# Kernel optimization log

Measured on AMD Instinct MI355X. Metric: run time of the kernel, lower is better.

The kernel has to match this reference:

```python
import jax, jax.numpy as jnp
import numpy as np

HEADS = 4
DIM_HEAD = 128

def setup_inputs() -> dict:
    key = jax.random.key(0)
    k1, k2, k3, k4 = jax.random.split(key, 4)
    scale = DIM_HEAD ** -0.5
    return {
        "fmap": jax.random.normal(k1, (16, 512, 32, 32), dtype=jnp.float32),
        "w_qkv": jax.random.normal(k2, (1536, 512), dtype=jnp.float32) * 0.02,
        "height": jax.random.normal(k3, (32, DIM_HEAD), dtype=jnp.float32) * scale,
        "width": jax.random.normal(k4, (32, DIM_HEAD), dtype=jnp.float32) * scale,
    }

def reference(fmap, w_qkv, height, width):
    b, c, h, w = fmap.shape
    scale = DIM_HEAD ** -0.5
    # 1x1 conv == channel GEMM: (b, 3*heads*dim_head, h, w)
    qkv = jnp.einsum('bchw,oc->bohw', fmap, w_qkv)
    # split into q,k,v and reshape to (b, heads, seq, dim_head)
    qkv = qkv.reshape(b, 3, HEADS, DIM_HEAD, h * w)
    q, k, v = (jnp.transpose(qkv[:, i], (0, 1, 3, 2)) for i in range(3))
    # content logits
    sim = jnp.einsum('bhid,bhjd->bhij', q, k) * scale
    # absolute positional bias: emb[(x,y)] = height[x] + width[y]
    emb = (height[:, None, :] + width[None, :, :]).reshape(h * w, DIM_HEAD)
    sim = sim + jnp.einsum('bhid,jd->bhij', q, emb) * scale
    attn = jax.nn.softmax(sim, axis=-1)
    out = jnp.einsum('bhij,bhjd->bhid', attn, v)  # (b, heads, seq, d)
    out = jnp.transpose(out, (0, 1, 3, 2)).reshape(b, HEADS * DIM_HEAD, h, w)
    return out
```

## Files before the change

kernel.cpp:

```cpp
#include <hip/hip_runtime.h>
#include <math.h>

#define HEADS 4
#define DIMH  128
#define NB    16
#define CIN   512
#define SEQ   1024
#define OTOT  1536

typedef __attribute__((ext_vector_type(8)))  short bf16x8;
typedef __attribute__((ext_vector_type(4)))  short bf16x4;
typedef __attribute__((ext_vector_type(4)))  float f32x4;
typedef __attribute__((ext_vector_type(16))) float f32x16;

#define MFMA16(a,b,c) __builtin_amdgcn_mfma_f32_16x16x32_bf16(a,b,c,0,0,0)
#define MFMA32(a,b,c) __builtin_amdgcn_mfma_f32_32x32x16_bf16(a,b,c,0,0,0)

#define GLOAD16(g, s) __builtin_amdgcn_global_load_lds( \
    (const __attribute__((address_space(1))) unsigned int*)(g), \
    (__attribute__((address_space(3))) unsigned int*)(s), 16, 0, 0)

__device__ __forceinline__ short f2bf(float f) {
    unsigned u = __builtin_bit_cast(unsigned, f);
    u = (u + 0x7FFFu + ((u >> 16) & 1u)) >> 16;
    return (short)u;
}

__global__ __launch_bounds__(256) void convert_fmap(const float* __restrict__ F,
                                                    short* __restrict__ FT) {
    __shared__ float tile[32][33];
    const int b = blockIdx.z, c0 = blockIdx.y * 32, s0 = blockIdx.x * 32;
    const int t = threadIdx.x;
    #pragma unroll
    for (int p = 0; p < 4; ++p) {
        int c = (t >> 5) + p * 8, s = t & 31;
        tile[c][s] = F[((size_t)b * CIN + c0 + c) * SEQ + s0 + s];
    }
    __syncthreads();
    #pragma unroll
    for (int p = 0; p < 2; ++p) {
        int s = (t >> 4) + p * 16, c2 = (t & 15) * 2;
        unsigned lo = (unsigned short)f2bf(tile[c2][s]);
        unsigned hi = (unsigned short)f2bf(tile[c2 + 1][s]);
        *(unsigned*)&FT[((size_t)b * SEQ + s0 + s) * CIN + c0 + c2] = lo | (hi << 16);
    }
}

__global__ __launch_bounds__(256) void convert_w(const float* __restrict__ W,
                                                 short* __restrict__ Wb) {
    int i = (blockIdx.x * 256 + threadIdx.x) * 4;
    float4 v = *(const float4*)&W[i];
    bf16x4 pk = { f2bf(v.x), f2bf(v.y), f2bf(v.z), f2bf(v.w) };
    *(bf16x4*)&Wb[i] = pk;
}

__global__ __launch_bounds__(256) void qkv_gemm(
    const short* __restrict__ Wb, const short* __restrict__ FT,
    const float* __restrict__ height, const float* __restrict__ width,
    short* __restrict__ Qo, short* __restrict__ Ko, short* __restrict__ Vo)
{
    __shared__ short As[128 * 32];
    __shared__ short Bs[128 * 32];
    const int b = blockIdx.z, o0 = blockIdx.y * 128, s0 = blockIdx.x * 128;
    const int t = threadIdx.x, l = t & 63, w = t >> 6;
    const int quad = l >> 4, ln = l & 15;
    const int wrow = (w >> 1) * 64, wcol = (w & 1) * 64;

    const short* Ablk = Wb + (size_t)o0 * CIN;
    const short* Bblk = FT + ((size_t)b * SEQ + s0) * CIN;

    f32x4 acc[4][4] = {};

    const int lrow = l >> 2, lcol = (l & 3) * 8;

    for (int k0 = 0; k0 < CIN; k0 += 32) {
        __syncthreads();
        {
            const short* gA = Ablk + (size_t)(w * 32 + lrow) * CIN + k0 + lcol;
            GLOAD16(gA,            As + (w * 32) * 32);
            GLOAD16(gA + 16 * CIN, As + (w * 32 + 16) * 32);
            const short* gB = Bblk + (size_t)(w * 32 + lrow) * CIN + k0 + lcol;
            GLOAD16(gB,            Bs + (w * 32) * 32);
            GLOAD16(gB + 16 * CIN, Bs + (w * 32 + 16) * 32);
        }
        __syncthreads();
        bf16x8 af[4], bfr[4];
        #pragma unroll
        for (int i = 0; i < 4; ++i)
            af[i] = *(const bf16x8*)&As[(wrow + i * 16 + ln) * 32 + quad * 8];
        #pragma unroll
        for (int j = 0; j < 4; ++j)
            bfr[j] = *(const bf16x8*)&Bs[(wcol + j * 16 + ln) * 32 + quad * 8];
        #pragma unroll
        for (int i = 0; i < 4; ++i)
            #pragma unroll
            for (int j = 0; j < 4; ++j)
                acc[i][j] = MFMA16(af[i], bfr[j], acc[i][j]);
    }

    const int sec = o0 >> 9;
    const int h   = (o0 >> 7) & 3;
    const size_t bh = (size_t)b * HEADS + h;

    if (sec == 0) {
        const float qs = 0.08838834764831845f * 1.4426950408889634f;
        #pragma unroll
        for (int ti = 0; ti < 4; ++ti) {
            int d = wrow + ti * 16 + quad * 4;
            #pragma unroll
            for (int tj = 0; tj < 4; ++tj) {
                int s = s0 + wcol + tj * 16 + ln;
                f32x4 a = acc[ti][tj];
                bf16x4 pk = { f2bf(a[0] * qs), f2bf(a[1] * qs), f2bf(a[2] * qs), f2bf(a[3] * qs) };
                *(bf16x4*)&Qo[(bh * SEQ + s) * DIMH + d] = pk;
            }
        }
    } else if (sec == 1) {
        #pragma unroll
        for (int ti = 0; ti < 4; ++ti) {
            int d = wrow + ti * 16 + quad * 4;
            #pragma unroll
            for (int tj = 0; tj < 4; ++tj) {
                int s = s0 + wcol + tj * 16 + ln;
                float4 hv = *(const float4*)&height[(size_t)(s >> 5) * DIMH + d];
                float4 wv = *(const float4*)&width[(size_t)(s & 31) * DIMH + d];
                f32x4 a = acc[ti][tj];
                bf16x4 pk = { f2bf(a[0] + hv.x + wv.x), f2bf(a[1] + hv.y + wv.y),
                              f2bf(a[2] + hv.z + wv.z), f2bf(a[3] + hv.w + wv.w) };
                *(bf16x4*)&Ko[(bh * SEQ + s) * DIMH + d] = pk;
            }
        }
    } else {
        #pragma unroll
        for (int ti = 0; ti < 4; ++ti) {
            int d = wrow + ti * 16 + quad * 4;
            #pragma unroll
            for (int tj = 0; tj < 4; ++tj) {
                int s = s0 + wcol + tj * 16 + ln;
                f32x4 a = acc[ti][tj];
                #pragma unroll
                for (int r = 0; r < 4; ++r)
                    Vo[(bh * DIMH + d + r) * SEQ + s] = f2bf(a[r]);
            }
        }
    }
}

#define BQ 128
#define BJ 64
#define KSTR 136
#define VSTR 72
#define PSTR 72

__global__ __launch_bounds__(256, 2) void attn(
    const short* __restrict__ Q, const short* __restrict__ K,
    const short* __restrict__ V, float* __restrict__ out)
{
    __shared__ short Ks[BJ * KSTR];
    __shared__ short Vs[DIMH * VSTR];
    __shared__ short Ps[BQ * PSTR];
    __shared__ float ls[BQ];

    const int t = threadIdx.x, l = t & 63, w = t >> 6;
    const int h = l >> 5, c31 = l & 31;

    const int L = blockIdx.x;
    const int x = L & 7, inner = L >> 3;
    const int bh = x * 8 + (inner >> 3);
    const int q0 = (inner & 7) * BQ;
    const size_t base = (size_t)bh * DIMH * SEQ;

    bf16x8 qf[8];
    {
        const short* Qp = Q + base + (size_t)(q0 + w * 32 + c31) * DIMH + h * 8;
        #pragma unroll
        for (int kc = 0; kc < 8; ++kc)
            qf[kc] = *(const bf16x8*)(Qp + kc * 16);
    }

    f32x16 O[4] = {};
    f32x16 psum = {};

    for (int j0 = 0; j0 < SEQ; j0 += BJ) {
        __syncthreads();
        #pragma unroll
        for (int p = 0; p < 4; ++p) {
            int j = (w * 4 + p) * 4 + (l >> 4);
            int c8 = (l & 15) * 8;
            int4 v = *(const int4*)(K + base + (size_t)(j0 + j) * DIMH + c8);
            *(int4*)&Ks[j * KSTR + c8] = v;
        }
        #pragma unroll
        for (int p = 0; p < 4; ++p) {
            int d = (w * 4 + p) * 8 + (l >> 3);
            int j8 = (l & 7) * 8;
            int4 v = *(const int4*)(V + base + (size_t)d * SEQ + j0 + j8);
            *(int4*)&Vs[d * VSTR + j8] = v;
        }
        __syncthreads();

        f32x16 S0 = {}, S1 = {};
        #pragma unroll
        for (int kc = 0; kc < 8; ++kc) {
            bf16x8 k0 = *(const bf16x8*)&Ks[c31 * KSTR + kc * 16 + h * 8];
            bf16x8 k1 = *(const bf16x8*)&Ks[(32 + c31) * KSTR + kc * 16 + h * 8];
            S0 = MFMA32(qf[kc], k0, S0);
            S1 = MFMA32(qf[kc], k1, S1);
        }

        #pragma unroll
        for (int r = 0; r < 16; ++r) {
            float p0 = __builtin_amdgcn_exp2f(S0[r]);
            float p1 = __builtin_amdgcn_exp2f(S1[r]);
            psum[r] += p0 + p1;
            int i = w * 32 + (r & 3) + 8 * (r >> 2) + 4 * h;
            Ps[i * PSTR + c31]      = f2bf(p0);
            Ps[i * PSTR + 32 + c31] = f2bf(p1);
        }

        #pragma unroll
        for (int jc = 0; jc < 4; ++jc) {
            bf16x8 pf = *(const bf16x8*)&Ps[(w * 32 + c31) * PSTR + jc * 16 + h * 8];
            #pragma unroll
            for (int dc = 0; dc < 4; ++dc) {
                bf16x8 vf = *(const bf16x8*)&Vs[(dc * 32 + c31) * VSTR + jc * 16 + h * 8];
                O[dc] = MFMA32(vf, pf, O[dc]);
            }
        }
    }

    #pragma unroll
    for (int r = 0; r < 16; ++r) {
        float s = psum[r];
        #pragma unroll
        for (int m = 1; m < 32; m <<= 1) s += __shfl_xor(s, m);
        psum[r] = s;
    }
    if (c31 == 0) {
        #pragma unroll
        for (int r = 0; r < 16; ++r)
            ls[w * 32 + (r & 3) + 8 * (r >> 2) + 4 * h] = psum[r];
    }
    float linv = 1.0f / ls[w * 32 + c31];

    #pragma unroll
    for (int dc = 0; dc < 4; ++dc)
        #pragma unroll
        for (int r = 0; r < 16; ++r) {
            int d = dc * 32 + (r & 3) + 8 * (r >> 2) + 4 * h;
            out[base + (size_t)d * SEQ + q0 + w * 32 + c31] = O[dc][r] * linv;
        }
}

extern "C" void kernel_launch(void* const* d_in, const int* in_sizes, int n_in,
                              void* d_out, int out_size, void* d_ws, size_t ws_size,
                              hipStream_t stream) {
    const float* fmap   = (const float*)d_in[0];
    const float* w_qkv  = (const float*)d_in[1];
    const float* height = (const float*)d_in[2];
    const float* width  = (const float*)d_in[3];
    float* outp = (float*)d_out;

    const size_t n_ft  = (size_t)NB * SEQ * CIN;
    const size_t n_w   = (size_t)OTOT * CIN;
    const size_t n_qkv = (size_t)NB * HEADS * SEQ * DIMH;

    short* FT = (short*)d_ws;
    short* Wb = FT + n_ft;
    short* Qb = Wb + n_w;
    short* Kb = Qb + n_qkv;
    short* Vb = Kb + n_qkv;

    convert_fmap<<<dim3(SEQ / 32, CIN / 32, NB), 256, 0, stream>>>(fmap, FT);
    convert_w<<<dim3(n_w / 1024), 256, 0, stream>>>(w_qkv, Wb);
    qkv_gemm<<<dim3(SEQ / 128, OTOT / 128, NB), 256, 0, stream>>>(
        Wb, FT, height, width, Qb, Kb, Vb);
    attn<<<dim3(NB * HEADS * (SEQ / BQ)), 256, 0, stream>>>(Qb, Kb, Vb, outp);
}
```

Baseline: 183.7 us.

## Pre-pack GEMM operands in k-octet layout and load MFMA fragments directly from global

The fmap and weight conversion kernels now write bf16 data in a [k/8][row][8] interleaved layout, so each lane's MFMA fragment is one contiguous 16-byte global load. The QKV GEMM drops its LDS staging and barriers and reads fragments straight from global memory, with a launch-bounds occupancy hint and a partially unrolled k loop. This removes LDS traffic and the two syncs per k-step. The cost is no data reuse through shared memory, so every wave fetches its own A/B fragments from L2 or HBM. Latency hiding now depends on occupancy and the unrolling alone.

Result: faster. 177.9 us (-3.2%).

```diff
diff --git a/kernel.cpp b/kernel.cpp
--- a/kernel.cpp
+++ b/kernel.cpp
@@ -7,6 +7,7 @@
 #define CIN   512
 #define SEQ   1024
 #define OTOT  1536
+#define KQ    (CIN / 8)
 
 typedef __attribute__((ext_vector_type(8)))  short bf16x8;
 typedef __attribute__((ext_vector_type(4)))  short bf16x4;
@@ -16,81 +17,60 @@
 #define MFMA16(a,b,c) __builtin_amdgcn_mfma_f32_16x16x32_bf16(a,b,c,0,0,0)
 #define MFMA32(a,b,c) __builtin_amdgcn_mfma_f32_32x32x16_bf16(a,b,c,0,0,0)
 
-#define GLOAD16(g, s) __builtin_amdgcn_global_load_lds( \
-    (const __attribute__((address_space(1))) unsigned int*)(g), \
-    (__attribute__((address_space(3))) unsigned int*)(s), 16, 0, 0)
-
 __device__ __forceinline__ short f2bf(float f) {
     unsigned u = __builtin_bit_cast(unsigned, f);
     u = (u + 0x7FFFu + ((u >> 16) & 1u)) >> 16;
     return (short)u;
 }
 
+__global__ __launch_bounds__(256) void convert_w(const float* __restrict__ W,
+                                                 short* __restrict__ Wb2) {
+    const int o  = blockIdx.x * 256 + threadIdx.x;
+    const int kq = blockIdx.y;
+    float4 v0 = *(const float4*)&W[(size_t)o * CIN + kq * 8];
+    float4 v1 = *(const float4*)&W[(size_t)o * CIN + kq * 8 + 4];
+    bf16x8 pk = { f2bf(v0.x), f2bf(v0.y), f2bf(v0.z), f2bf(v0.w),
+                  f2bf(v1.x), f2bf(v1.y), f2bf(v1.z), f2bf(v1.w) };
+    *(bf16x8*)&Wb2[((size_t)kq * OTOT + o) * 8] = pk;
+}
+
 __global__ __launch_bounds__(256) void convert_fmap(const float* __restrict__ F,
-                                                    short* __restrict__ FT) {
-    __shared__ float tile[32][33];
-    const int b = blockIdx.z, c0 = blockIdx.y * 32, s0 = blockIdx.x * 32;
-    const int t = threadIdx.x;
+                                                    short* __restrict__ FT2) {
+    const int s  = blockIdx.x * 256 + threadIdx.x;
+    const int kq = blockIdx.y, b = blockIdx.z;
+    const float* src = F + ((size_t)b * CIN + kq * 8) * SEQ + s;
+    float v[8];
     #pragma unroll
-    for (int p = 0; p < 4; ++p) {
-        int c = (t >> 5) + p * 8, s = t & 31;
-        tile[c][s] = F[((size_t)b * CIN + c0 + c) * SEQ + s0 + s];
-    }
-    __syncthreads();
-    #pragma unroll
-    for (int p = 0; p < 2; ++p) {
-        int s = (t >> 4) + p * 16, c2 = (t & 15) * 2;
-        unsigned lo = (unsigned short)f2bf(tile[c2][s]);
-        unsigned hi = (unsigned short)f2bf(tile[c2 + 1][s]);
-        *(unsigned*)&FT[((size_t)b * SEQ + s0 + s) * CIN + c0 + c2] = lo | (hi << 16);
-    }
-}
-
-__global__ __launch_bounds__(256) void convert_w(const float* __restrict__ W,
-                                                 short* __restrict__ Wb) {
-    int i = (blockIdx.x * 256 + threadIdx.x) * 4;
-    float4 v = *(const float4*)&W[i];
-    bf16x4 pk = { f2bf(v.x), f2bf(v.y), f2bf(v.z), f2bf(v.w) };
-    *(bf16x4*)&Wb[i] = pk;
-}
-
-__global__ __launch_bounds__(256) void qkv_gemm(
-    const short* __restrict__ Wb, const short* __restrict__ FT,
+    for (int i = 0; i < 8; ++i) v[i] = src[(size_t)i * SEQ];
+    bf16x8 pk = { f2bf(v[0]), f2bf(v[1]), f2bf(v[2]), f2bf(v[3]),
+                  f2bf(v[4]), f2bf(v[5]), f2bf(v[6]), f2bf(v[7]) };
+    *(bf16x8*)&FT2[(((size_t)b * KQ + kq) * SEQ + s) * 8] = pk;
+}
+
+__global__ __launch_bounds__(256, 3) void qkv_gemm(
+    const short* __restrict__ Wb2, const short* __restrict__ FT2,
     const float* __restrict__ height, const float* __restrict__ width,
     short* __restrict__ Qo, short* __restrict__ Ko, short* __restrict__ Vo)
 {
-    __shared__ short As[128 * 32];
-    __shared__ short Bs[128 * 32];
     const int b = blockIdx.z, o0 = blockIdx.y * 128, s0 = blockIdx.x * 128;
     const int t = threadIdx.x, l = t & 63, w = t >> 6;
     const int quad = l >> 4, ln = l & 15;
     const int wrow = (w >> 1) * 64, wcol = (w & 1) * 64;
 
-    const short* Ablk = Wb + (size_t)o0 * CIN;
-    const short* Bblk = FT + ((size_t)b * SEQ + s0) * CIN;
+    const short* Ap = Wb2 + (((size_t)quad * OTOT) + (o0 + wrow + ln)) * 8;
+    const short* Bp = FT2 + ((((size_t)b * KQ + quad) * SEQ) + (s0 + wcol + ln)) * 8;
 
     f32x4 acc[4][4] = {};
 
-    const int lrow = l >> 2, lcol = (l & 3) * 8;
-
-    for (int k0 = 0; k0 < CIN; k0 += 32) {
-        __syncthreads();
-        {
-            const short* gA = Ablk + (size_t)(w * 32 + lrow) * CIN + k0 + lcol;
-            GLOAD16(gA,            As + (w * 32) * 32);
-            GLOAD16(gA + 16 * CIN, As + (w * 32 + 16) * 32);
-            const short* gB = Bblk + (size_t)(w * 32 + lrow) * CIN + k0 + lcol;
-            GLOAD16(gB,            Bs + (w * 32) * 32);
-            GLOAD16(gB + 16 * CIN, Bs + (w * 32 + 16) * 32);
-        }
-        __syncthreads();
+    #pragma unroll 2
+    for (int ks = 0; ks < 16; ++ks) {
         bf16x8 af[4], bfr[4];
-        #pragma unroll
-        for (int i = 0; i < 4; ++i)
-            af[i] = *(const bf16x8*)&As[(wrow + i * 16 + ln) * 32 + quad * 8];
-        #pragma unroll
-        for (int j = 0; j < 4; ++j)
-            bfr[j] = *(const bf16x8*)&Bs[(wcol + j * 16 + ln) * 32 + quad * 8];
+        const short* a = Ap + (size_t)ks * 4 * OTOT * 8;
+        const short* bb = Bp + (size_t)ks * 4 * SEQ * 8;
+        #pragma unroll
+        for (int i = 0; i < 4; ++i) af[i] = *(const bf16x8*)(a + (size_t)i * 16 * 8);
+        #pragma unroll
+        for (int j = 0; j < 4; ++j) bfr[j] = *(const bf16x8*)(bb + (size_t)j * 16 * 8);
         #pragma unroll
         for (int i = 0; i < 4; ++i)
             #pragma unroll
@@ -265,15 +245,15 @@
     const size_t n_w   = (size_t)OTOT * CIN;
     const size_t n_qkv = (size_t)NB * HEADS * SEQ * DIMH;
 
-    short* FT = (short*)d_ws;
-    short* Wb = FT + n_ft;
-    short* Qb = Wb + n_w;
-    short* Kb = Qb + n_qkv;
-    short* Vb = Kb + n_qkv;
-
-    convert_fmap<<<dim3(SEQ / 32, CIN / 32, NB), 256, 0, stream>>>(fmap, FT);
-    convert_w<<<dim3(n_w / 1024), 256, 0, stream>>>(w_qkv, Wb);
+    short* FT2 = (short*)d_ws;
+    short* Wb2 = FT2 + n_ft;
+    short* Qb  = Wb2 + n_w;
+    short* Kb  = Qb + n_qkv;
+    short* Vb  = Kb + n_qkv;
+
+    convert_fmap<<<dim3(SEQ / 256, KQ, NB), 256, 0, stream>>>(fmap, FT2);
+    convert_w<<<dim3(OTOT / 256, KQ), 256, 0, stream>>>(w_qkv, Wb2);
     qkv_gemm<<<dim3(SEQ / 128, OTOT / 128, NB), 256, 0, stream>>>(
-        Wb, FT, height, width, Qb, Kb, Vb);
+        Wb2, FT2, height, width, Qb, Kb, Vb);
     attn<<<dim3(NB * HEADS * (SEQ / BQ)), 256, 0, stream>>>(Qb, Kb, Vb, outp);
 }
```
